# Kernel optimization log

Measured on AMD Instinct MI355X. Metric: run time of the kernel, lower is better.

Reference implementation:

```python
import jax, jax.numpy as jnp
import numpy as np

EMBED = 512
HEADS = 8
HEAD_DIM = EMBED // HEADS


def setup_inputs() -> dict:
    key = jax.random.key(0)
    kv, kk, kq, kw, kb = jax.random.split(key, 5)
    N, S = 2, 4096
    values = jax.random.normal(kv, (N, S, EMBED), dtype=jnp.float32)
    keys = jax.random.normal(kk, (N, S, EMBED), dtype=jnp.float32)
    query = jax.random.normal(kq, (N, S, EMBED), dtype=jnp.float32)
    # fc_out: Linear(embed, embed) with bias (only linear actually used in forward)
    bound = 1.0 / np.sqrt(EMBED)
    fc_w = jax.random.uniform(kw, (EMBED, EMBED), minval=-bound, maxval=bound, dtype=jnp.float32)
    fc_b = jax.random.uniform(kb, (EMBED,), minval=-bound, maxval=bound, dtype=jnp.float32)
    return {"values": values, "keys": keys, "query": query, "fc_w": fc_w, "fc_b": fc_b}


def reference(values, keys, query, fc_w, fc_b):
    N, S_q, _ = query.shape
    S_kv = keys.shape[1]
    # NOTE: source defines q/k/v Linear layers but never applies them; raw inputs are reshaped.
    v = values.reshape(N, S_kv, HEADS, HEAD_DIM)
    k = keys.reshape(N, S_kv, HEADS, HEAD_DIM)
    q = query.reshape(N, S_q, HEADS, HEAD_DIM)
    energy = jnp.einsum("nqhd,nkhd->nhqk", q, k)  # [N,H,Sq,Skv] -- full attention matrix
    attn = jax.nn.softmax(energy / jnp.sqrt(jnp.float32(EMBED)), axis=3)
    out = jnp.einsum("nhql,nlhd->nqhd", attn, v).reshape(N, S_q, EMBED)
    # fc_out: x @ W.T + b (torch Linear convention)
    return out @ fc_w.T + fc_b
```

## Files before the change

### kernel.cpp

```cpp
#include <hip/hip_runtime.h>
#include <hip/hip_bf16.h>

#define SEQ    4096
#define EMBED  512
#define NHEAD  8
#define HD     64
#define NBATCH 2
#define NT     (SEQ / 128)
#define SCALE2 0.06376390773f

typedef __bf16 bf16_t;
typedef bf16_t bf16x8 __attribute__((ext_vector_type(8)));
typedef float  f32x16 __attribute__((ext_vector_type(16)));
typedef float  f32x4  __attribute__((ext_vector_type(4)));
typedef unsigned short u16_t;
typedef u16_t  u16x8  __attribute__((ext_vector_type(8)));
typedef unsigned int u32_t;
typedef u32_t  u32x4  __attribute__((ext_vector_type(4)));

static __device__ __forceinline__ u16_t f2bfu(float f) {
    return __builtin_bit_cast(u16_t, (__bf16)f);
}
static __device__ __forceinline__ u32_t pk(float lo, float hi) {
    return (u32_t)f2bfu(lo) | ((u32_t)f2bfu(hi) << 16);
}
static __device__ __forceinline__ void plswap(u32_t& a, u32_t& b) {
    asm("v_permlane32_swap_b32 %0, %1" : "+v"(a), "+v"(b));
}
static __device__ __forceinline__ f32x16 mfma32(bf16x8 a, bf16x8 b, f32x16 c) {
    return __builtin_amdgcn_mfma_f32_32x32x16_bf16(a, b, c, 0, 0, 0);
}
static __device__ __forceinline__ f32x4 mfma16(bf16x8 a, bf16x8 b, f32x4 c) {
    return __builtin_amdgcn_mfma_f32_16x16x32_bf16(a, b, c, 0, 0, 0);
}
static __device__ __forceinline__ bf16x8 rd8(const u16_t* p, int idx) {
    return __builtin_bit_cast(bf16x8, *reinterpret_cast<const u16x8*>(p + idx));
}
static __device__ __forceinline__ void gload16(const u16_t* g, u16_t* l) {
    __builtin_amdgcn_global_load_lds(
        (const __attribute__((address_space(1))) unsigned int*)g,
        (__attribute__((address_space(3))) unsigned int*)l, 16, 0, 0);
}
static __device__ __forceinline__ u16x8 pack8(float4 f0, float4 f1) {
    u16x8 u;
    u[0] = f2bfu(f0.x); u[1] = f2bfu(f0.y); u[2] = f2bfu(f0.z); u[3] = f2bfu(f0.w);
    u[4] = f2bfu(f1.x); u[5] = f2bfu(f1.y); u[6] = f2bfu(f1.z); u[7] = f2bfu(f1.w);
    return u;
}

__global__ __launch_bounds__(256)
void prep_q(const float* __restrict__ Q, u16_t* __restrict__ Qb)
{
    const size_t idx = ((size_t)blockIdx.x * 256 + threadIdx.x) * 8;
    float4 f0 = *reinterpret_cast<const float4*>(Q + idx);
    float4 f1 = *reinterpret_cast<const float4*>(Q + idx + 4);
    f0.x *= SCALE2; f0.y *= SCALE2; f0.z *= SCALE2; f0.w *= SCALE2;
    f1.x *= SCALE2; f1.y *= SCALE2; f1.z *= SCALE2; f1.w *= SCALE2;
    *reinterpret_cast<u16x8*>(Qb + idx) = pack8(f0, f1);
}

__global__ __launch_bounds__(256)
void prep_kv(const float* __restrict__ K, const float* __restrict__ V,
             u16_t* __restrict__ Kf, u16_t* __restrict__ Vf)
{
    __shared__ u16_t T[64 * 80];

    const int s0 = blockIdx.x * 64;
    const int h  = blockIdx.y;
    const int n  = blockIdx.z;
    const int tid = threadIdx.x;
    const int key = tid >> 2;
    const int c0  = (tid & 3) * 16;

    const size_t nh = (size_t)n * NHEAD + h;
    u16_t* kt_ = Kf + nh * ((size_t)SEQ * HD) + (size_t)blockIdx.x * 4096;
    u16_t* vt_ = Vf + nh * ((size_t)SEQ * HD) + (size_t)blockIdx.x * 4096;

    {
        const float* kp = K + ((size_t)(n * SEQ + s0 + key)) * EMBED + h * HD + c0;
        float4 f0 = *reinterpret_cast<const float4*>(kp);
        float4 f1 = *reinterpret_cast<const float4*>(kp + 4);
        float4 f2 = *reinterpret_cast<const float4*>(kp + 8);
        float4 f3 = *reinterpret_cast<const float4*>(kp + 12);
        const int ks = c0 >> 4;
        *reinterpret_cast<u16x8*>(&kt_[ks * 1024 + key * 8])       = pack8(f0, f1);
        *reinterpret_cast<u16x8*>(&kt_[ks * 1024 + 512 + key * 8]) = pack8(f2, f3);
    }
    {
        const float* vp = V + ((size_t)(n * SEQ + s0 + key)) * EMBED + h * HD + c0;
        float4 f0 = *reinterpret_cast<const float4*>(vp);
        float4 f1 = *reinterpret_cast<const float4*>(vp + 4);
        float4 f2 = *reinterpret_cast<const float4*>(vp + 8);
        float4 f3 = *reinterpret_cast<const float4*>(vp + 12);
        *reinterpret_cast<u16x8*>(&T[key * 80 + c0])     = pack8(f0, f1);
        *reinterpret_cast<u16x8*>(&T[key * 80 + c0 + 8]) = pack8(f2, f3);
    }
    __syncthreads();
#pragma unroll
    for (int cc = 0; cc < 2; ++cc) {
        const int ch = tid + cc * 256;
        const int ks = ch >> 7;
        const int hf = (ch >> 6) & 1;
        const int d  = ch & 63;
        u16x8 g;
#pragma unroll
        for (int j = 0; j < 8; ++j) g[j] = T[(ks * 16 + hf * 8 + j) * 80 + d];
        *reinterpret_cast<u16x8*>(&vt_[ks * 1024 + hf * 512 + d * 8]) = g;
    }
}

__global__ __launch_bounds__(512, 4)
void attn_fwd(const u16_t* __restrict__ Qb, const u16_t* __restrict__ Kf,
              const u16_t* __restrict__ Vf, u16_t* __restrict__ Xout)
{
    __shared__ __align__(16) u16_t SMK[2][8192];
    __shared__ __align__(16) u16_t SMV[2][8192];
    __shared__ float Lbuf[2][4][32];

    const int qt   = blockIdx.x;
    const int head = blockIdx.y;
    const int n    = blockIdx.z;
    const int tid  = threadIdx.x;
    const int wave = tid >> 6;
    const int lane = tid & 63;
    const int qg   = wave & 3;
    const int kg   = wave >> 2;
    const int hf   = lane >> 5;
    const int l31  = lane & 31;

    const size_t nh = (size_t)n * NHEAD + head;
    const u16_t* kLane = Kf + nh * ((size_t)SEQ * HD) + wave * 1024 + lane * 8;
    const u16_t* vLane = Vf + nh * ((size_t)SEQ * HD) + wave * 1024 + lane * 8;

    bf16x8 qf[4];
    {
        const int qrow = qt * 128 + qg * 32 + l31;
        const u16_t* qp = Qb + ((size_t)n * SEQ + qrow) * EMBED + head * HD + hf * 8;
#pragma unroll
        for (int ks = 0; ks < 4; ++ks) qf[ks] = rd8(qp, ks * 16);
    }

    f32x16 o[2];
#pragma unroll
    for (int dt = 0; dt < 2; ++dt)
#pragma unroll
        for (int r = 0; r < 16; ++r) o[dt][r] = 0.f;
    float lsum = 0.f;

    const int fbase = kg * 4096 + hf * 512 + l31 * 8;

    {
        gload16(kLane,       &SMK[0][wave * 1024]);
        gload16(kLane + 512, &SMK[0][wave * 1024 + 512]);
        gload16(vLane,       &SMV[0][wave * 1024]);
        gload16(vLane + 512, &SMV[0][wave * 1024 + 512]);
    }

    auto stage = [&](int kt, int buf) {
        const u16_t* ks_ = kLane + (size_t)kt * 8192;
        const u16_t* vs_ = vLane + (size_t)kt * 8192;
        gload16(ks_,       &SMK[buf][wave * 1024]);
        gload16(ks_ + 512, &SMK[buf][wave * 1024 + 512]);
        gload16(vs_,       &SMV[buf][wave * 1024]);
        gload16(vs_ + 512, &SMV[buf][wave * 1024 + 512]);
    };

    auto compute = [&](const u16_t* Kt, const u16_t* Vt) {
        u32x4 pa[4];
#pragma unroll
        for (int t = 0; t < 2; ++t) {
            bf16x8 kf0 = rd8(Kt, fbase + 0 * 1024 + t * 256);
            bf16x8 kf1 = rd8(Kt, fbase + 1 * 1024 + t * 256);
            bf16x8 kf2 = rd8(Kt, fbase + 2 * 1024 + t * 256);
            bf16x8 kf3 = rd8(Kt, fbase + 3 * 1024 + t * 256);
            f32x16 z;
#pragma unroll
            for (int r = 0; r < 16; ++r) z[r] = 0.f;
            __builtin_amdgcn_s_setprio(1);
            z = mfma32(kf0, qf[0], z);
            z = mfma32(kf1, qf[1], z);
            z = mfma32(kf2, qf[2], z);
            z = mfma32(kf3, qf[3], z);
            __builtin_amdgcn_s_setprio(0);

            float p[16];
#pragma unroll
            for (int r = 0; r < 16; ++r) p[r] = __builtin_amdgcn_exp2f(z[r]);
            float rs = 0.f;
#pragma unroll
            for (int r = 0; r < 16; ++r) rs += p[r];
            lsum += rs;

            u32_t a0 = pk(p[0],  p[1]),  b0 = pk(p[4],  p[5]);
            u32_t a1 = pk(p[2],  p[3]),  b1 = pk(p[6],  p[7]);
            u32_t a2 = pk(p[8],  p[9]),  b2 = pk(p[12], p[13]);
            u32_t a3 = pk(p[10], p[11]), b3 = pk(p[14], p[15]);
            plswap(a0, b0); plswap(a1, b1); plswap(a2, b2); plswap(a3, b3);
            pa[2 * t + 0][0] = a0; pa[2 * t + 0][1] = a1;
            pa[2 * t + 0][2] = b0; pa[2 * t + 0][3] = b1;
            pa[2 * t + 1][0] = a2; pa[2 * t + 1][1] = a3;
            pa[2 * t + 1][2] = b2; pa[2 * t + 1][3] = b3;
        }

        __builtin_amdgcn_s_setprio(1);
#pragma unroll
        for (int dt = 0; dt < 2; ++dt) {
            bf16x8 vf0 = rd8(Vt, fbase + 0 * 1024 + dt * 256);
            bf16x8 vf1 = rd8(Vt, fbase + 1 * 1024 + dt * 256);
            bf16x8 vf2 = rd8(Vt, fbase + 2 * 1024 + dt * 256);
            bf16x8 vf3 = rd8(Vt, fbase + 3 * 1024 + dt * 256);
            o[dt] = mfma32(__builtin_bit_cast(bf16x8, pa[0]), vf0, o[dt]);
            o[dt] = mfma32(__builtin_bit_cast(bf16x8, pa[1]), vf1, o[dt]);
            o[dt] = mfma32(__builtin_bit_cast(bf16x8, pa[2]), vf2, o[dt]);
            o[dt] = mfma32(__builtin_bit_cast(bf16x8, pa[3]), vf3, o[dt]);
        }
        __builtin_amdgcn_s_setprio(0);
    };

#pragma unroll 1
    for (int ktp = 0; ktp < NT / 2; ++ktp) {
        __syncthreads();
        stage(2 * ktp + 1, 1);
        compute(SMK[0], SMV[0]);
        __syncthreads();
        if (ktp < NT / 2 - 1) stage(2 * ktp + 2, 0);
        compute(SMK[1], SMV[1]);
    }

    const float lf = lsum + __shfl_xor(lsum, 32);

    __syncthreads();

#define CROW(r) ((((r) & 3) + 8 * ((r) >> 2)) + 4 * hf)
    float* Ob = (float*)SMK + qg * 2048;
    if (kg == 1) {
#pragma unroll
        for (int dt = 0; dt < 2; ++dt)
#pragma unroll
            for (int r = 0; r < 16; ++r)
                Ob[CROW(r) * 64 + dt * 32 + l31] = o[dt][r];
        if (lane < 32) Lbuf[1][qg][l31] = lf;
    } else {
        if (lane < 32) Lbuf[0][qg][l31] = lf;
    }
    __syncthreads();
    if (kg == 0) {
#pragma unroll
        for (int r = 0; r < 16; ++r) {
            const int q = CROW(r);
            const float linv = 1.f / (Lbuf[0][qg][q] + Lbuf[1][qg][q]);
            const int grow = qt * 128 + qg * 32 + q;
            u16_t* xp = Xout + ((size_t)n * SEQ + grow) * EMBED + head * HD;
#pragma unroll
            for (int dt = 0; dt < 2; ++dt) {
                const float v = (o[dt][r] + Ob[q * 64 + dt * 32 + l31]) * linv;
                xp[dt * 32 + l31] = f2bfu(v);
            }
        }
    }
#undef CROW
}

__global__ __launch_bounds__(256)
void fc_gemm(const u16_t* __restrict__ X, const float* __restrict__ Wg,
             const float* __restrict__ Bg, float* __restrict__ Y)
{
    __shared__ __align__(16) u16_t Xlds[64 * 64];
    __shared__ __align__(16) u16_t Wlds[64 * 64];

    const int mt = blockIdx.x, nt = blockIdx.y;
    const int tid = threadIdx.x;
    const int wave = tid >> 6, lane = tid & 63;
    const int lg = lane >> 4, l15 = lane & 15;

    f32x4 acc[4];
#pragma unroll
    for (int cg = 0; cg < 4; ++cg) acc[cg] = (f32x4){0.f, 0.f, 0.f, 0.f};

    const int sr  = tid >> 2;
    const int sc0 = (tid & 3) * 16;

    for (int kk = 0; kk < EMBED / 64; ++kk) {
        const int k0 = kk * 64;
        {
            const u16_t* xp = X + ((size_t)(mt * 64 + sr)) * EMBED + k0 + sc0;
#pragma unroll
            for (int b = 0; b < 2; ++b) {
                u16x8 u = *reinterpret_cast<const u16x8*>(xp + b * 8);
                *reinterpret_cast<u16x8*>(&Xlds[sr * 64 + ((sc0 + b * 8) ^ ((sr & 7) << 3))]) = u;
            }
        }
        {
            const float* wp = Wg + ((size_t)(nt * 64 + sr)) * EMBED + k0 + sc0;
#pragma unroll
            for (int b = 0; b < 2; ++b) {
                float4 f0 = *reinterpret_cast<const float4*>(wp + b * 8);
                float4 f1 = *reinterpret_cast<const float4*>(wp + b * 8 + 4);
                *reinterpret_cast<u16x8*>(&Wlds[sr * 64 + ((sc0 + b * 8) ^ ((sr & 7) << 3))]) =
                    pack8(f0, f1);
            }
        }
        __syncthreads();

        bf16x8 ax0, ax1;
        {
            const int xr = wave * 16 + l15;
            ax0 = rd8(Xlds, xr * 64 + ((lg * 8)      ^ ((xr & 7) << 3)));
            ax1 = rd8(Xlds, xr * 64 + ((32 + lg * 8) ^ ((xr & 7) << 3)));
        }
#pragma unroll
        for (int cg = 0; cg < 4; ++cg) {
            const int wr = cg * 16 + l15;
            bf16x8 w0 = rd8(Wlds, wr * 64 + ((lg * 8)      ^ ((wr & 7) << 3)));
            bf16x8 w1 = rd8(Wlds, wr * 64 + ((32 + lg * 8) ^ ((wr & 7) << 3)));
            acc[cg] = mfma16(ax0, w0, acc[cg]);
            acc[cg] = mfma16(ax1, w1, acc[cg]);
        }
        __syncthreads();
    }

#pragma unroll
    for (int cg = 0; cg < 4; ++cg)
#pragma unroll
        for (int i = 0; i < 4; ++i) {
            const int m  = mt * 64 + wave * 16 + lg * 4 + i;
            const int nn = nt * 64 + cg * 16 + l15;
            Y[(size_t)m * EMBED + nn] = acc[cg][i] + Bg[nn];
        }
}

extern "C" void kernel_launch(void* const* d_in, const int* in_sizes, int n_in,
                              void* d_out, int out_size, void* d_ws, size_t ws_size,
                              hipStream_t stream)
{
    const float* Vg = (const float*)d_in[0];
    const float* Kg = (const float*)d_in[1];
    const float* Qg = (const float*)d_in[2];
    const float* Wg = (const float*)d_in[3];
    const float* Bg = (const float*)d_in[4];
    float* Y = (float*)d_out;

    const size_t NSE = (size_t)NBATCH * SEQ * EMBED;
    u16_t* Qb = (u16_t*)d_ws;
    u16_t* Kf = Qb + NSE;
    u16_t* Vf = Kf + NSE;
    u16_t* Xw = Vf + NSE;

    prep_q<<<dim3(NSE / (256 * 8)), 256, 0, stream>>>(Qg, Qb);
    prep_kv<<<dim3(SEQ / 64, NHEAD, NBATCH), 256, 0, stream>>>(Kg, Vg, Kf, Vf);

    attn_fwd<<<dim3(SEQ / 128, NHEAD, NBATCH), 512, 0, stream>>>(Qb, Kf, Vf, Xw);

    fc_gemm<<<dim3((NBATCH * SEQ) / 64, EMBED / 64), 256, 0, stream>>>(Xw, Wg, Bg, Y);
}
```

Baseline: 119.1 us.

## Split attention into 64-row query tiles with 4-way key split and single V buffer

Halves the query tile per block to 64 rows, so the launch grows from 512 to 1024 blocks, and splits each key tile four ways across waves. A 1D grid swizzle spreads the (batch, head) pairs across the grid. Shared memory drops to two K buffers plus one V buffer, loaded in stages with a partial vmcnt wait and barrier between QK and PV, which allows more resident blocks (launch bounds raised to 6). The cost is K/V traffic doubled per query row, more barriers per tile, and a 4-way cross-wave reduction of outputs and row sums at the end.

```diff
diff --git a/kernel.cpp b/kernel.cpp
--- a/kernel.cpp
+++ b/kernel.cpp
@@ -109,32 +109,38 @@
     }
 }
 
-__global__ __launch_bounds__(512, 4)
+__global__ __launch_bounds__(512, 6)
 void attn_fwd(const u16_t* __restrict__ Qb, const u16_t* __restrict__ Kf,
               const u16_t* __restrict__ Vf, u16_t* __restrict__ Xout)
 {
-    __shared__ __align__(16) u16_t SMK[2][8192];
-    __shared__ __align__(16) u16_t SMV[2][8192];
-    __shared__ float Lbuf[2][4][32];
-
-    const int qt   = blockIdx.x;
-    const int head = blockIdx.y;
-    const int n    = blockIdx.z;
+    __shared__ __align__(16) u16_t SM[3 * 8192];
+    __shared__ float Lbuf[4][2][32];
+
+    u16_t* const KB0 = SM;
+    u16_t* const KB1 = SM + 8192;
+    u16_t* const VB  = SM + 16384;
+
+    const int bid = blockIdx.x;
+    const int idx = bid >> 3;
+    const int nh  = (bid & 7) * 2 + (idx >> 6);
+    const int qt  = idx & 63;
+    const int head = nh & 7;
+    const int n    = nh >> 3;
+
     const int tid  = threadIdx.x;
     const int wave = tid >> 6;
     const int lane = tid & 63;
-    const int qg   = wave & 3;
-    const int kg   = wave >> 2;
+    const int qg   = wave >> 2;
+    const int kg   = wave & 3;
     const int hf   = lane >> 5;
     const int l31  = lane & 31;
 
-    const size_t nh = (size_t)n * NHEAD + head;
-    const u16_t* kLane = Kf + nh * ((size_t)SEQ * HD) + wave * 1024 + lane * 8;
-    const u16_t* vLane = Vf + nh * ((size_t)SEQ * HD) + wave * 1024 + lane * 8;
+    const u16_t* kLane = Kf + (size_t)nh * SEQ * HD + wave * 1024 + lane * 8;
+    const u16_t* vLane = Vf + (size_t)nh * SEQ * HD + wave * 1024 + lane * 8;
 
     bf16x8 qf[4];
     {
-        const int qrow = qt * 128 + qg * 32 + l31;
+        const int qrow = qt * 64 + qg * 32 + l31;
         const u16_t* qp = Qb + ((size_t)n * SEQ + qrow) * EMBED + head * HD + hf * 8;
 #pragma unroll
         for (int ks = 0; ks < 4; ++ks) qf[ks] = rd8(qp, ks * 16);
@@ -147,113 +153,121 @@
         for (int r = 0; r < 16; ++r) o[dt][r] = 0.f;
     float lsum = 0.f;
 
-    const int fbase = kg * 4096 + hf * 512 + l31 * 8;
-
-    {
-        gload16(kLane,       &SMK[0][wave * 1024]);
-        gload16(kLane + 512, &SMK[0][wave * 1024 + 512]);
-        gload16(vLane,       &SMV[0][wave * 1024]);
-        gload16(vLane + 512, &SMV[0][wave * 1024 + 512]);
-    }
-
-    auto stage = [&](int kt, int buf) {
-        const u16_t* ks_ = kLane + (size_t)kt * 8192;
-        const u16_t* vs_ = vLane + (size_t)kt * 8192;
-        gload16(ks_,       &SMK[buf][wave * 1024]);
-        gload16(ks_ + 512, &SMK[buf][wave * 1024 + 512]);
-        gload16(vs_,       &SMV[buf][wave * 1024]);
-        gload16(vs_ + 512, &SMV[buf][wave * 1024 + 512]);
+    const int fK = (kg >> 1) * 4096 + (kg & 1) * 256  + hf * 512 + l31 * 8;
+    const int fV = (kg >> 1) * 4096 + (kg & 1) * 2048 + hf * 512 + l31 * 8;
+
+    gload16(kLane,       KB0 + wave * 1024);
+    gload16(kLane + 512, KB0 + wave * 1024 + 512);
+
+    auto stageV = [&](int kt) {
+        const u16_t* vs = vLane + (size_t)kt * 8192;
+        gload16(vs,       VB + wave * 1024);
+        gload16(vs + 512, VB + wave * 1024 + 512);
     };
-
-    auto compute = [&](const u16_t* Kt, const u16_t* Vt) {
-        u32x4 pa[4];
-#pragma unroll
-        for (int t = 0; t < 2; ++t) {
-            bf16x8 kf0 = rd8(Kt, fbase + 0 * 1024 + t * 256);
-            bf16x8 kf1 = rd8(Kt, fbase + 1 * 1024 + t * 256);
-            bf16x8 kf2 = rd8(Kt, fbase + 2 * 1024 + t * 256);
-            bf16x8 kf3 = rd8(Kt, fbase + 3 * 1024 + t * 256);
-            f32x16 z;
-#pragma unroll
-            for (int r = 0; r < 16; ++r) z[r] = 0.f;
-            __builtin_amdgcn_s_setprio(1);
-            z = mfma32(kf0, qf[0], z);
-            z = mfma32(kf1, qf[1], z);
-            z = mfma32(kf2, qf[2], z);
-            z = mfma32(kf3, qf[3], z);
-            __builtin_amdgcn_s_setprio(0);
-
-            float p[16];
-#pragma unroll
-            for (int r = 0; r < 16; ++r) p[r] = __builtin_amdgcn_exp2f(z[r]);
-            float rs = 0.f;
-#pragma unroll
-            for (int r = 0; r < 16; ++r) rs += p[r];
-            lsum += rs;
-
-            u32_t a0 = pk(p[0],  p[1]),  b0 = pk(p[4],  p[5]);
-            u32_t a1 = pk(p[2],  p[3]),  b1 = pk(p[6],  p[7]);
-            u32_t a2 = pk(p[8],  p[9]),  b2 = pk(p[12], p[13]);
-            u32_t a3 = pk(p[10], p[11]), b3 = pk(p[14], p[15]);
-            plswap(a0, b0); plswap(a1, b1); plswap(a2, b2); plswap(a3, b3);
-            pa[2 * t + 0][0] = a0; pa[2 * t + 0][1] = a1;
-            pa[2 * t + 0][2] = b0; pa[2 * t + 0][3] = b1;
-            pa[2 * t + 1][0] = a2; pa[2 * t + 1][1] = a3;
-            pa[2 * t + 1][2] = b2; pa[2 * t + 1][3] = b3;
-        }
-
+    auto stageK = [&](int kt, u16_t* kb) {
+        const u16_t* ks = kLane + (size_t)(kt & (NT - 1)) * 8192;
+        gload16(ks,       kb + wave * 1024);
+        gload16(ks + 512, kb + wave * 1024 + 512);
+    };
+
+    auto computeQK = [&](const u16_t* Kt, u32x4* pa) {
+        bf16x8 k0 = rd8(Kt, fK);
+        bf16x8 k1 = rd8(Kt, fK + 1024);
+        bf16x8 k2 = rd8(Kt, fK + 2048);
+        bf16x8 k3 = rd8(Kt, fK + 3072);
+        f32x16 z;
+#pragma unroll
+        for (int r = 0; r < 16; ++r) z[r] = 0.f;
         __builtin_amdgcn_s_setprio(1);
-#pragma unroll
-        for (int dt = 0; dt < 2; ++dt) {
-            bf16x8 vf0 = rd8(Vt, fbase + 0 * 1024 + dt * 256);
-            bf16x8 vf1 = rd8(Vt, fbase + 1 * 1024 + dt * 256);
-            bf16x8 vf2 = rd8(Vt, fbase + 2 * 1024 + dt * 256);
-            bf16x8 vf3 = rd8(Vt, fbase + 3 * 1024 + dt * 256);
-            o[dt] = mfma32(__builtin_bit_cast(bf16x8, pa[0]), vf0, o[dt]);
-            o[dt] = mfma32(__builtin_bit_cast(bf16x8, pa[1]), vf1, o[dt]);
-            o[dt] = mfma32(__builtin_bit_cast(bf16x8, pa[2]), vf2, o[dt]);
-            o[dt] = mfma32(__builtin_bit_cast(bf16x8, pa[3]), vf3, o[dt]);
-        }
+        z = mfma32(k0, qf[0], z);
+        z = mfma32(k1, qf[1], z);
+        z = mfma32(k2, qf[2], z);
+        z = mfma32(k3, qf[3], z);
+        __builtin_amdgcn_s_setprio(0);
+
+        float p[16];
+#pragma unroll
+        for (int r = 0; r < 16; ++r) p[r] = __builtin_amdgcn_exp2f(z[r]);
+        float rs = 0.f;
+#pragma unroll
+        for (int r = 0; r < 16; ++r) rs += p[r];
+        lsum += rs;
+
+        u32_t a0 = pk(p[0],  p[1]),  b0 = pk(p[4],  p[5]);
+        u32_t a1 = pk(p[2],  p[3]),  b1 = pk(p[6],  p[7]);
+        u32_t a2 = pk(p[8],  p[9]),  b2 = pk(p[12], p[13]);
+        u32_t a3 = pk(p[10], p[11]), b3 = pk(p[14], p[15]);
+        plswap(a0, b0); plswap(a1, b1); plswap(a2, b2); plswap(a3, b3);
+        pa[0][0] = a0; pa[0][1] = a1; pa[0][2] = b0; pa[0][3] = b1;
+        pa[1][0] = a2; pa[1][1] = a3; pa[1][2] = b2; pa[1][3] = b3;
+    };
+
+    auto computePV = [&](const u32x4* pa) {
+        bf16x8 v00 = rd8(VB, fV);
+        bf16x8 v01 = rd8(VB, fV + 256);
+        bf16x8 v10 = rd8(VB, fV + 1024);
+        bf16x8 v11 = rd8(VB, fV + 1024 + 256);
+        __builtin_amdgcn_s_setprio(1);
+        o[0] = mfma32(__builtin_bit_cast(bf16x8, pa[0]), v00, o[0]);
+        o[0] = mfma32(__builtin_bit_cast(bf16x8, pa[1]), v10, o[0]);
+        o[1] = mfma32(__builtin_bit_cast(bf16x8, pa[0]), v01, o[1]);
+        o[1] = mfma32(__builtin_bit_cast(bf16x8, pa[1]), v11, o[1]);
         __builtin_amdgcn_s_setprio(0);
     };
 
 #pragma unroll 1
-    for (int ktp = 0; ktp < NT / 2; ++ktp) {
+    for (int kt2 = 0; kt2 < NT / 2; ++kt2) {
+        const int kt = kt2 * 2;
+        u32x4 pa[2];
+
         __syncthreads();
-        stage(2 * ktp + 1, 1);
-        compute(SMK[0], SMV[0]);
+        stageV(kt);
+        stageK(kt + 1, KB1);
+        computeQK(KB0, pa);
+        asm volatile("s_waitcnt vmcnt(2)" ::: "memory");
+        __builtin_amdgcn_s_barrier();
+        __builtin_amdgcn_sched_barrier(0);
+        computePV(pa);
+
         __syncthreads();
-        if (ktp < NT / 2 - 1) stage(2 * ktp + 2, 0);
-        compute(SMK[1], SMV[1]);
+        stageV(kt + 1);
+        stageK(kt + 2, KB0);
+        computeQK(KB1, pa);
+        asm volatile("s_waitcnt vmcnt(2)" ::: "memory");
+        __builtin_amdgcn_s_barrier();
+        __builtin_amdgcn_sched_barrier(0);
+        computePV(pa);
     }
 
     const float lf = lsum + __shfl_xor(lsum, 32);
-
+    if (lane < 32) Lbuf[kg][qg][l31] = lf;
     __syncthreads();
 
 #define CROW(r) ((((r) & 3) + 8 * ((r) >> 2)) + 4 * hf)
-    float* Ob = (float*)SMK + qg * 2048;
-    if (kg == 1) {
+    float* OB = (float*)SM;
+    if (kg != 0) {
+        float* Ob = OB + ((kg - 1) * 2 + qg) * 2048;
 #pragma unroll
         for (int dt = 0; dt < 2; ++dt)
 #pragma unroll
             for (int r = 0; r < 16; ++r)
                 Ob[CROW(r) * 64 + dt * 32 + l31] = o[dt][r];
-        if (lane < 32) Lbuf[1][qg][l31] = lf;
-    } else {
-        if (lane < 32) Lbuf[0][qg][l31] = lf;
     }
     __syncthreads();
     if (kg == 0) {
 #pragma unroll
         for (int r = 0; r < 16; ++r) {
             const int q = CROW(r);
-            const float linv = 1.f / (Lbuf[0][qg][q] + Lbuf[1][qg][q]);
-            const int grow = qt * 128 + qg * 32 + q;
+            const float linv = 1.f / (Lbuf[0][qg][q] + Lbuf[1][qg][q] +
+                                      Lbuf[2][qg][q] + Lbuf[3][qg][q]);
+            const int grow = qt * 64 + qg * 32 + q;
             u16_t* xp = Xout + ((size_t)n * SEQ + grow) * EMBED + head * HD;
 #pragma unroll
             for (int dt = 0; dt < 2; ++dt) {
-                const float v = (o[dt][r] + Ob[q * 64 + dt * 32 + l31]) * linv;
+                const float v = (o[dt][r]
+                                 + OB[(0 * 2 + qg) * 2048 + q * 64 + dt * 32 + l31]
+                                 + OB[(1 * 2 + qg) * 2048 + q * 64 + dt * 32 + l31]
+                                 + OB[(2 * 2 + qg) * 2048 + q * 64 + dt * 32 + l31]) * linv;
                 xp[dt * 32 + l31] = f2bfu(v);
             }
         }
@@ -349,7 +363,7 @@
     prep_q<<<dim3(NSE / (256 * 8)), 256, 0, stream>>>(Qg, Qb);
     prep_kv<<<dim3(SEQ / 64, NHEAD, NBATCH), 256, 0, stream>>>(Kg, Vg, Kf, Vf);
 
-    attn_fwd<<<dim3(SEQ / 128, NHEAD, NBATCH), 512, 0, stream>>>(Qb, Kf, Vf, Xw);
+    attn_fwd<<<dim3(1024), 512, 0, stream>>>(Qb, Kf, Vf, Xw);
 
     fc_gemm<<<dim3((NBATCH * SEQ) / 64, EMBED / 64), 256, 0, stream>>>(Xw, Wg, Bg, Y);
 }
```

Result: slower. 203.9 us (+71.1%).
